# Performance work log

Measured on AMD Instinct MI355X. Metric: run time of the kernel, lower is better.

Reference implementation:

```python
import jax, jax.numpy as jnp
import numpy as np

TAU = 2.0
BN_EPS = 1e-5
HEADS = 8

# spikingjelly-style Heaviside spike with sigmoid surrogate gradient (alpha=4)
@jax.custom_vjp
def spike(x):
    return (x >= 0.0).astype(x.dtype)

def _spike_fwd(x):
    return (x >= 0.0).astype(x.dtype), x

def _spike_bwd(x, g):
    s = jax.nn.sigmoid(4.0 * x)
    return (g * 4.0 * s * (1.0 - s),)

spike.defvjp(_spike_fwd, _spike_bwd)

def lif(x, thresh):
    """Multi-step LIF (tau=2, decay_input=True, hard reset to 0, detach_reset).
    x: (T, ...) input current; returns spikes of the same shape."""
    def step(v, xt):
        v = v + (xt - v) / TAU          # charge
        s = spike(v - thresh)           # fire
        v = v * (1.0 - jax.lax.stop_gradient(s))  # hard reset, detached
        return v, s
    _, s = jax.lax.scan(step, jnp.zeros_like(x[0]), x)
    return s

def bn(x, gamma, beta, mean, var):
    # inference-mode BatchNorm2d over channel axis 2 of (T,B,C,H,W)
    sh = (1, 1, -1, 1, 1)
    scale = gamma / jnp.sqrt(var + BN_EPS)
    return (x - mean.reshape(sh)) * scale.reshape(sh) + beta.reshape(sh)

def setup_inputs() -> dict:
    key = jax.random.key(0)
    T, B, C, H, W = 4, 16, 512, 16, 16
    ks = jax.random.split(key, 24)
    def wmat(k):
        return jax.random.normal(k, (C, C), jnp.float32) * (1.0 / np.sqrt(C))
    def bnp(k):
        k1, k2, k3, k4 = jax.random.split(k, 4)
        return (jax.random.normal(k1, (C,), jnp.float32) * 0.1 + 1.0,
                jax.random.normal(k2, (C,), jnp.float32) * 0.1,
                jax.random.normal(k3, (C,), jnp.float32) * 0.1,
                jax.random.uniform(k4, (C,), jnp.float32) + 0.5)
    qg, qb, qm, qvar = bnp(ks[1]); kg, kb, km, kvar = bnp(ks[3])
    vg, vb, vm, vvar = bnp(ks[5]); pg, pb, pm, pvar = bnp(ks[8])
    return {
        'x': jax.random.normal(ks[0], (T, B, C, H, W), jnp.float32),
        'wq': wmat(ks[10]), 'qg': qg, 'qb': qb, 'qm': qm, 'qvar': qvar,
        'wk': wmat(ks[11]), 'kg': kg, 'kb': kb, 'km': km, 'kvar': kvar,
        'wv': wmat(ks[12]), 'vg': vg, 'vb': vb, 'vm': vm, 'vvar': vvar,
        'wp': wmat(ks[13]), 'bp': jax.random.normal(ks[14], (C,), jnp.float32) * 0.02,
        'pg': pg, 'pb': pb, 'pm': pm, 'pvar': pvar,
    }

def reference(x, wq, qg, qb, qm, qvar, wk, kg, kb, km, kvar,
              wv, vg, vb, vm, vvar, wp, bp, pg, pb, pm, pvar):
    T, B, C, H, W = x.shape
    dh = C // HEADS
    N = H * W
    identity = x
    xs = lif(x, 1.0)  # shortcut_lif

    def branch(w, g, b, m, v):
        y = jnp.einsum('tbchw,oc->tbohw', xs, w)  # 1x1 conv, no bias
        return lif(bn(y, g, b, m, v), 1.0)

    # (T,B,C,H,W) spikes -> (T,B,heads,N,dh)
    def to_heads(s):
        return s.reshape(T, B, HEADS, dh, N).transpose(0, 1, 2, 4, 3)

    q = to_heads(branch(wq, qg, qb, qm, qvar))
    k = to_heads(branch(wk, kg, kb, km, kvar))
    v = to_heads(branch(wv, vg, vb, vm, vvar))

    kv = (k * v).sum(axis=3, keepdims=True)   # sum over tokens N -> (T,B,h,1,dh)
    kv = lif(kv, 0.5)                          # talking_heads_lif (v_threshold=0.5)

    out = q * kv                               # (T,B,h,N,dh)
    out = out.transpose(0, 1, 2, 4, 3).reshape(T, B, C, H, W)
    out = jnp.einsum('tbchw,oc->tbohw', out, wp) + bp.reshape(1, 1, -1, 1, 1)
    out = bn(out, pg, pb, pm, pvar) + identity
    return out, v
```

## Files before the change

### kernel.cpp

```cpp
#include <hip/hip_runtime.h>
#include <hip/hip_bf16.h>

typedef unsigned short u16;
typedef unsigned int u32;
typedef __attribute__((ext_vector_type(8))) short bh8;
typedef __attribute__((ext_vector_type(4))) short sh4;
typedef __attribute__((ext_vector_type(4))) float f4;

#define T_   4
#define B_   16
#define C_   512
#define N_   256
#define M2_  4096

__device__ __forceinline__ u16 f2bf(float f) {
  u32 u = __float_as_uint(f);
  u32 r = (u + 0x7FFFu + ((u >> 16) & 1u)) >> 16;
  return (u16)r;
}
__device__ __forceinline__ void gl_lds16(const void* g, void* l) {
  __builtin_amdgcn_global_load_lds(
      (const __attribute__((address_space(1))) unsigned int*)g,
      (__attribute__((address_space(3))) unsigned int*)l, 16, 0, 0);
}

__global__ void k_prep_lif(const float* __restrict__ x, u16* __restrict__ xs,
                           const float* __restrict__ wq, const float* __restrict__ wk,
                           const float* __restrict__ wv, const float* __restrict__ wp,
                           const float* qg, const float* qb, const float* qm, const float* qv,
                           const float* kg, const float* kb, const float* km, const float* kv2,
                           const float* vg, const float* vb, const float* vm, const float* vv,
                           const float* pg, const float* pb, const float* pm, const float* pv,
                           const float* bp,
                           u16* __restrict__ wcat, u16* __restrict__ wpcat,
                           float* bns, float* pss) {
  __shared__ u16 sp[4][64][68];
  int bid = blockIdx.x;
  int tid = threadIdx.x;
  if (bid < 512) {
    int b = bid >> 5, c0 = ((bid >> 2) & 7) * 64, n0 = (bid & 3) * 64;
    int rq = tid >> 4;
    int n4 = (tid & 15) * 4;
    float v[16];
#pragma unroll
    for (int i = 0; i < 16; i++) v[i] = 0.f;
    for (int t = 0; t < 4; t++) {
      const float* xb = x + (((size_t)t * 16 + b) * 512 + c0) * 256 + n0;
#pragma unroll
      for (int i = 0; i < 4; i++) {
        int row = rq + i * 16;
        f4 xv = *(const f4*)(xb + (size_t)row * 256 + n4);
        sh4 sv;
#pragma unroll
        for (int j = 0; j < 4; j++) {
          float vv2 = v[i * 4 + j];
          vv2 = vv2 + (xv[j] - vv2) * 0.5f;
          u16 s = 0;
          if (vv2 >= 1.0f) { s = 0x3F80; vv2 = 0.f; }
          v[i * 4 + j] = vv2;
          sv[j] = (short)s;
        }
        *(sh4*)&sp[t][row][n4] = sv;
      }
    }
    __syncthreads();
    int cp = (tid & 31) * 2;
    int nq = tid >> 5;
    for (int t = 0; t < 4; t++) {
      u16* ob = xs + (((size_t)t * 16 + b) * 256 + n0) * 512 + c0;
#pragma unroll
      for (int i = 0; i < 8; i++) {
        int n = nq + i * 8;
        u32 w = (u32)sp[t][cp][n] | ((u32)sp[t][cp + 1][n] << 16);
        *(u32*)(ob + (size_t)n * 512 + cp) = w;
      }
    }
  } else {
    int id = (bid - 512) * 256 + tid;
    if (id < 1048576) {
      int mat = id >> 18;
      int rc  = id & 262143;
      int o = rc >> 9, c = rc & 511;
      const float* src = (mat == 0) ? wq : (mat == 1) ? wk : (mat == 2) ? wv : wp;
      float w = src[rc];
      u16 hu = f2bf(w);
      float hf = __uint_as_float(((u32)hu) << 16);
      u16 lu = f2bf(w - hf);
      if (mat < 3) {
        size_t base = ((size_t)(mat * 512 + o)) * 1024 + c;
        wcat[base] = hu; wcat[base + 512] = lu;
      } else {
        size_t base = (size_t)o * 1024 + c;
        wpcat[base] = hu; wpcat[base + 512] = lu;
      }
    } else {
      int j = id - 1048576;
      if (j < 1536) {
        int br = j >> 9, c = j & 511;
        const float *g, *b, *m, *va;
        if (br == 0)      { g = qg; b = qb; m = qm; va = qv; }
        else if (br == 1) { g = kg; b = kb; m = km; va = kv2; }
        else              { g = vg; b = vb; m = vm; va = vv; }
        float s = g[c] / sqrtf(va[c] + 1e-5f);
        bns[j * 4 + 0] = s; bns[j * 4 + 1] = m[c]; bns[j * 4 + 2] = b[c];
        bns[j * 4 + 3] = 0.f;
      } else if (j < 2048) {
        int c = j - 1536;
        float s = pg[c] / sqrtf(pv[c] + 1e-5f);
        pss[c * 4 + 0] = bp[c]; pss[c * 4 + 1] = pm[c];
        pss[c * 4 + 2] = s;     pss[c * 4 + 3] = pb[c];
      }
    }
  }
}

__launch_bounds__(256, 2)
__global__ void k_qkv_gemm(const u16* __restrict__ xs, const u16* __restrict__ wcat,
                           const float* __restrict__ bns,
                           u16* __restrict__ qs, u16* __restrict__ kvsp) {
  __shared__ char lds[81920];
  int tid = threadIdx.x, lane = tid & 63, wid = tid >> 6;
  int wr = wid >> 1, wc = wid & 1, lr = lane & 15, lq = lane >> 4;
  int m0 = blockIdx.x * 128, o0 = blockIdx.y * 96;

  float scl[3], mn[3], bt[3];
#pragma unroll
  for (int ni = 0; ni < 3; ni++) {
    int ch = o0 + wc * 48 + ni * 16 + lr;
    scl[ni] = bns[ch * 4]; mn[ni] = bns[ch * 4 + 1]; bt[ni] = bns[ch * 4 + 2];
  }

  int srow = tid >> 3;
  u32 sgoff = (u32)(((tid & 7) ^ (srow & 7)) << 4);
  u32 ldst = (u32)tid * 16;

  u32 aoff[4], boff[3];
#pragma unroll
  for (int mi = 0; mi < 4; mi++) {
    int r = wr * 64 + mi * 16 + lr;
    aoff[mi] = r * 128 + ((lq ^ (r & 7)) << 4);
  }
#pragma unroll
  for (int ni = 0; ni < 3; ni++) {
    int r = wc * 48 + ni * 16 + lr;
    boff[ni] = r * 128 + ((lq ^ (r & 7)) << 4);
  }

  const char* Bb = (const char*)wcat + (size_t)o0 * 2048;

  auto STAGE = [&](int buf, int step) {
    int t = step >> 3;
    u32 kb = (u32)(step & 7) * 128;
    const char* Ab = (const char*)xs + ((size_t)t * M2_ + m0) * 1024;
    char* L = lds + buf * 40960;
#pragma unroll
    for (int r2 = 0; r2 < 4; r2++)
      gl_lds16(Ab + (size_t)(r2 * 32 + srow) * 1024 + kb + sgoff, L + r2 * 4096 + ldst);
#pragma unroll
    for (int r2 = 0; r2 < 3; r2++) {
      gl_lds16(Bb + (size_t)(r2 * 32 + srow) * 2048 + kb + sgoff, L + 16384 + r2 * 4096 + ldst);
      gl_lds16(Bb + (size_t)(r2 * 32 + srow) * 2048 + 1024 + kb + sgoff, L + 28672 + r2 * 4096 + ldst);
    }
  };

  float vst[4][3][4];
#pragma unroll
  for (int a = 0; a < 4; a++)
#pragma unroll
    for (int b = 0; b < 3; b++)
#pragma unroll
      for (int c = 0; c < 4; c++) vst[a][b][c] = 0.f;

  f4 acc[4][3];
  STAGE(0, 0);
  __syncthreads();
  int cur = 0;
  for (int step = 0; step < 32; ++step) {
    int ks = step & 7;
    if (ks == 0) {
#pragma unroll
      for (int a = 0; a < 4; a++)
#pragma unroll
        for (int b = 0; b < 3; b++) { acc[a][b][0] = 0.f; acc[a][b][1] = 0.f; acc[a][b][2] = 0.f; acc[a][b][3] = 0.f; }
    }
    if (step < 31) STAGE(cur ^ 1, step + 1);
    const char* L = lds + cur * 40960;
#pragma unroll
    for (int h = 0; h < 2; h++) {
      u32 hx = (u32)h << 6;
      bh8 af[4], bf[3], lf[3];
#pragma unroll
      for (int mi = 0; mi < 4; mi++)
        af[mi] = *(const bh8*)(L + (aoff[mi] ^ hx));
#pragma unroll
      for (int ni = 0; ni < 3; ni++) {
        bf[ni] = *(const bh8*)(L + 16384 + (boff[ni] ^ hx));
        lf[ni] = *(const bh8*)(L + 28672 + (boff[ni] ^ hx));
      }
#pragma unroll
      for (int mi = 0; mi < 4; mi++)
#pragma unroll
        for (int ni = 0; ni < 3; ni++)
          acc[mi][ni] = __builtin_amdgcn_mfma_f32_16x16x32_bf16(af[mi], bf[ni], acc[mi][ni], 0, 0, 0);
#pragma unroll
      for (int mi = 0; mi < 4; mi++)
#pragma unroll
        for (int ni = 0; ni < 3; ni++)
          acc[mi][ni] = __builtin_amdgcn_mfma_f32_16x16x32_bf16(af[mi], lf[ni], acc[mi][ni], 0, 0, 0);
    }
    asm volatile("s_waitcnt vmcnt(0)" ::: "memory");
    __builtin_amdgcn_s_barrier();
    cur ^= 1;
    if (ks == 7) {
      int t = step >> 3;
#pragma unroll
      for (int mi = 0; mi < 4; mi++)
#pragma unroll
        for (int ni = 0; ni < 3; ni++)
#pragma unroll
          for (int j = 0; j < 4; j++) {
            float y = acc[mi][ni][j];
            y = (y - mn[ni]) * scl[ni] + bt[ni];
            float vv = vst[mi][ni][j];
            vv = vv + (y - vv) * 0.5f;
            u16 s = 0;
            if (vv >= 1.0f) { s = 0x3F80; vv = 0.f; }
            vst[mi][ni][j] = vv;
            int rg = m0 + wr * 64 + mi * 16 + lq * 4 + j;
            int o = o0 + wc * 48 + ni * 16 + lr;
            size_t rowg = (size_t)t * M2_ + rg;
            if (o < 512) qs[rowg * 512 + o] = s;
            else         kvsp[rowg * 1024 + (o - 512)] = s;
          }
    }
  }
}

__global__ void k_kvv(const u16* __restrict__ kvsp, float* __restrict__ vout,
                      int* __restrict__ kvp) {
  int tb = blockIdx.x >> 3, nc = blockIdx.x & 7;
  int tid = threadIdx.x;
  const char* base = (const char*)kvsp + ((size_t)tb * 256 + nc * 32) * 2048;
  int c = tid * 2, h = c >> 6, d = c & 63;
  float* vo = vout + (((size_t)tb * 8 + h) * 256 + nc * 32) * 64 + d;
  int cnt0 = 0, cnt1 = 0;
  for (int n = 0; n < 32; n++) {
    u32 kk = *(const u32*)(base + (size_t)n * 2048 + c * 2);
    u32 vv = *(const u32*)(base + (size_t)n * 2048 + 1024 + c * 2);
    u32 a = kk & vv;
    cnt0 += (a & 0xFFFFu) ? 1 : 0;
    cnt1 += (a >> 16) ? 1 : 0;
    float2 w;
    w.x = (vv & 0xFFFFu) ? 1.f : 0.f;
    w.y = (vv >> 16) ? 1.f : 0.f;
    *(float2*)(vo + (size_t)n * 64) = w;
  }
  kvp[((tb * 8 + nc) << 9) + c]     = cnt0;
  kvp[((tb * 8 + nc) << 9) + c + 1] = cnt1;
}

__global__ void k_tlif(const int* __restrict__ kvp, unsigned char* __restrict__ mask) {
  int id = blockIdx.x * 256 + threadIdx.x;
  int b = id >> 9, c = id & 511;
  float v = 0.f;
  for (int t = 0; t < 4; t++) {
    int tb = t * 16 + b;
    int s = 0;
#pragma unroll
    for (int nc = 0; nc < 8; nc++) s += kvp[((tb * 8 + nc) << 9) + c];
    float xx = (float)s;
    v = v + (xx - v) * 0.5f;
    unsigned char sp = 0;
    if (v >= 0.5f) { sp = 1; v = 0.f; }
    mask[tb * 512 + c] = sp;
  }
}

__launch_bounds__(256, 2)
__global__ void k_proj_gemm(const u16* __restrict__ qs, const unsigned char* __restrict__ mask,
                            const u16* __restrict__ wpc, const float* __restrict__ pss,
                            const float* __restrict__ x, float* __restrict__ out) {
  __shared__ char lds[66560];
  u16* lm = (u16*)(lds + 65536);
  int tid = threadIdx.x, lane = tid & 63, wid = tid >> 6;
  int wr = wid >> 1, wc = wid & 1, lr = lane & 15, lq = lane >> 4;
  int m0 = blockIdx.x * 128, o0 = blockIdx.y * 64;
  int tb = m0 >> 8;

  lm[tid]       = mask[tb * 512 + tid]       ? (u16)0xFFFF : (u16)0;
  lm[tid + 256] = mask[tb * 512 + tid + 256] ? (u16)0xFFFF : (u16)0;

  int srow = tid >> 3;
  u32 sgoff = (u32)(((tid & 7) ^ (srow & 7)) << 4);
  u32 ldst = (u32)tid * 16;

  u32 aoff[4], boff[2];
#pragma unroll
  for (int mi = 0; mi < 4; mi++) {
    int r = wr * 64 + mi * 16 + lr;
    aoff[mi] = r * 128 + ((lq ^ (r & 7)) << 4);
  }
#pragma unroll
  for (int ni = 0; ni < 2; ni++) {
    int r = wc * 32 + ni * 16 + lr;
    boff[ni] = r * 128 + ((lq ^ (r & 7)) << 4);
  }

  const char* Ab = (const char*)qs + (size_t)m0 * 1024;
  const char* Bb = (const char*)wpc + (size_t)o0 * 2048;

  auto STAGE = [&](int buf, int step) {
    u32 kb = (u32)step * 128;
    char* L = lds + buf * 32768;
#pragma unroll
    for (int r2 = 0; r2 < 4; r2++)
      gl_lds16(Ab + (size_t)(r2 * 32 + srow) * 1024 + kb + sgoff, L + r2 * 4096 + ldst);
#pragma unroll
    for (int r2 = 0; r2 < 2; r2++) {
      gl_lds16(Bb + (size_t)(r2 * 32 + srow) * 2048 + kb + sgoff, L + 16384 + r2 * 4096 + ldst);
      gl_lds16(Bb + (size_t)(r2 * 32 + srow) * 2048 + 1024 + kb + sgoff, L + 24576 + r2 * 4096 + ldst);
    }
  };

  f4 acc[4][2];
#pragma unroll
  for (int a = 0; a < 4; a++)
#pragma unroll
    for (int b = 0; b < 2; b++) { acc[a][b][0] = 0.f; acc[a][b][1] = 0.f; acc[a][b][2] = 0.f; acc[a][b][3] = 0.f; }

  STAGE(0, 0);
  __syncthreads();
  int cur = 0;
  for (int step = 0; step < 8; ++step) {
    u32 kb = (u32)step * 128;
    if (step < 7) STAGE(cur ^ 1, step + 1);
    const char* L = lds + cur * 32768;
#pragma unroll
    for (int h = 0; h < 2; h++) {
      u32 hx = (u32)h << 6;
      bh8 mq = *(const bh8*)((const char*)lm + kb + (h << 6) + lq * 16);
      bh8 af[4], bf[2], lf[2];
#pragma unroll
      for (int mi = 0; mi < 4; mi++) {
        af[mi] = *(const bh8*)(L + (aoff[mi] ^ hx));
        af[mi] = af[mi] & mq;
      }
#pragma unroll
      for (int ni = 0; ni < 2; ni++) {
        bf[ni] = *(const bh8*)(L + 16384 + (boff[ni] ^ hx));
        lf[ni] = *(const bh8*)(L + 24576 + (boff[ni] ^ hx));
      }
#pragma unroll
      for (int mi = 0; mi < 4; mi++)
#pragma unroll
        for (int ni = 0; ni < 2; ni++)
          acc[mi][ni] = __builtin_amdgcn_mfma_f32_16x16x32_bf16(af[mi], bf[ni], acc[mi][ni], 0, 0, 0);
#pragma unroll
      for (int mi = 0; mi < 4; mi++)
#pragma unroll
        for (int ni = 0; ni < 2; ni++)
          acc[mi][ni] = __builtin_amdgcn_mfma_f32_16x16x32_bf16(af[mi], lf[ni], acc[mi][ni], 0, 0, 0);
    }
    asm volatile("s_waitcnt vmcnt(0)" ::: "memory");
    __builtin_amdgcn_s_barrier();
    cur ^= 1;
  }
#pragma unroll
  for (int mi = 0; mi < 4; mi++)
#pragma unroll
    for (int ni = 0; ni < 2; ni++) {
      int o = o0 + wc * 32 + ni * 16 + lr;
      f4 ps = *(const f4*)&pss[o * 4];
      int n = (m0 & 255) + wr * 64 + mi * 16 + lq * 4;
      size_t idx = (size_t)tb * 131072 + (size_t)o * 256 + n;
      f4 xv = *(const f4*)&x[idx];
      f4 res;
#pragma unroll
      for (int j = 0; j < 4; j++) {
        float u = acc[mi][ni][j] + ps[0];
        u = (u - ps[1]) * ps[2] + ps[3];
        res[j] = u + xv[j];
      }
      *(f4*)&out[idx] = res;
    }
}

extern "C" void kernel_launch(void* const* d_in, const int* in_sizes, int n_in,
                              void* d_out, int out_size, void* d_ws, size_t ws_size,
                              hipStream_t stream) {
  const float* x  = (const float*)d_in[0];
  const float* wq = (const float*)d_in[1];
  const float* qg = (const float*)d_in[2];
  const float* qb = (const float*)d_in[3];
  const float* qm = (const float*)d_in[4];
  const float* qv = (const float*)d_in[5];
  const float* wk = (const float*)d_in[6];
  const float* kg = (const float*)d_in[7];
  const float* kb = (const float*)d_in[8];
  const float* km = (const float*)d_in[9];
  const float* kv = (const float*)d_in[10];
  const float* wv = (const float*)d_in[11];
  const float* vg = (const float*)d_in[12];
  const float* vb = (const float*)d_in[13];
  const float* vm = (const float*)d_in[14];
  const float* vv = (const float*)d_in[15];
  const float* wp = (const float*)d_in[16];
  const float* bp = (const float*)d_in[17];
  const float* pg = (const float*)d_in[18];
  const float* pb = (const float*)d_in[19];
  const float* pm = (const float*)d_in[20];
  const float* pv = (const float*)d_in[21];

  char* w = (char*)d_ws;
  u16*  XS    = (u16*)(w + 0);
  u16*  QS    = (u16*)(w + 16777216);
  u16*  KVSP  = (u16*)(w + 33554432);
  u16*  WCAT  = (u16*)(w + 67108864);
  u16*  WPCAT = (u16*)(w + 70254592);
  float* BNS  = (float*)(w + 71303168);
  float* PSS  = (float*)(w + 71327744);
  int*   KVP  = (int*)(w + 71335936);
  unsigned char* MASK = (unsigned char*)(w + 72384512);

  float* out  = (float*)d_out;
  float* vout = out + 8388608;

  k_prep_lif<<<4616, 256, 0, stream>>>(x, XS, wq, wk, wv, wp,
                                       qg, qb, qm, qv, kg, kb, km, kv,
                                       vg, vb, vm, vv, pg, pb, pm, pv, bp,
                                       WCAT, WPCAT, BNS, PSS);
  k_qkv_gemm<<<dim3(32, 16), 256, 0, stream>>>(XS, WCAT, BNS, QS, KVSP);
  k_kvv<<<512, 256, 0, stream>>>(KVSP, vout, KVP);
  k_tlif<<<32, 256, 0, stream>>>(KVP, MASK);
  k_proj_gemm<<<dim3(128, 8), 256, 0, stream>>>(QS, MASK, WPCAT, PSS, x, out);
}
```

Before: 213.7 us.

## Fuse k*v token reduction and v output into QKV GEMM epilogue

Result: faster. 203.2 us (-4.9%).

```diff
diff --git a/kernel.cpp b/kernel.cpp
--- a/kernel.cpp
+++ b/kernel.cpp
@@ -41,20 +41,27 @@
     int b = bid >> 5, c0 = ((bid >> 2) & 7) * 64, n0 = (bid & 3) * 64;
     int rq = tid >> 4;
     int n4 = (tid & 15) * 4;
-    float v[16];
-#pragma unroll
-    for (int i = 0; i < 16; i++) v[i] = 0.f;
+    f4 xr[4][4];
+#pragma unroll
     for (int t = 0; t < 4; t++) {
       const float* xb = x + (((size_t)t * 16 + b) * 512 + c0) * 256 + n0;
 #pragma unroll
+      for (int i = 0; i < 4; i++)
+        xr[t][i] = *(const f4*)(xb + (size_t)(rq + i * 16) * 256 + n4);
+    }
+    float v[16];
+#pragma unroll
+    for (int i = 0; i < 16; i++) v[i] = 0.f;
+#pragma unroll
+    for (int t = 0; t < 4; t++) {
+#pragma unroll
       for (int i = 0; i < 4; i++) {
         int row = rq + i * 16;
-        f4 xv = *(const f4*)(xb + (size_t)row * 256 + n4);
         sh4 sv;
 #pragma unroll
         for (int j = 0; j < 4; j++) {
           float vv2 = v[i * 4 + j];
-          vv2 = vv2 + (xv[j] - vv2) * 0.5f;
+          vv2 = vv2 + (xr[t][i][j] - vv2) * 0.5f;
           u16 s = 0;
           if (vv2 >= 1.0f) { s = 0x3F80; vv2 = 0.f; }
           v[i * 4 + j] = vv2;
@@ -87,7 +94,8 @@
       float hf = __uint_as_float(((u32)hu) << 16);
       u16 lu = f2bf(w - hf);
       if (mat < 3) {
-        size_t base = ((size_t)(mat * 512 + o)) * 1024 + c;
+        int rI = (o >> 5) * 96 + mat * 32 + (o & 31);
+        size_t base = (size_t)rI * 1024 + c;
         wcat[base] = hu; wcat[base + 512] = lu;
       } else {
         size_t base = (size_t)o * 1024 + c;
@@ -96,14 +104,15 @@
     } else {
       int j = id - 1048576;
       if (j < 1536) {
-        int br = j >> 9, c = j & 511;
+        int br = j >> 9, o = j & 511;
         const float *g, *b, *m, *va;
         if (br == 0)      { g = qg; b = qb; m = qm; va = qv; }
         else if (br == 1) { g = kg; b = kb; m = km; va = kv2; }
         else              { g = vg; b = vb; m = vm; va = vv; }
-        float s = g[c] / sqrtf(va[c] + 1e-5f);
-        bns[j * 4 + 0] = s; bns[j * 4 + 1] = m[c]; bns[j * 4 + 2] = b[c];
-        bns[j * 4 + 3] = 0.f;
+        float s = g[o] / sqrtf(va[o] + 1e-5f);
+        int rI = (o >> 5) * 96 + br * 32 + (o & 31);
+        bns[rI * 4 + 0] = s; bns[rI * 4 + 1] = m[o]; bns[rI * 4 + 2] = b[o];
+        bns[rI * 4 + 3] = 0.f;
       } else if (j < 2048) {
         int c = j - 1536;
         float s = pg[c] / sqrtf(pv[c] + 1e-5f);
@@ -117,32 +126,37 @@
 __launch_bounds__(256, 2)
 __global__ void k_qkv_gemm(const u16* __restrict__ xs, const u16* __restrict__ wcat,
                            const float* __restrict__ bns,
-                           u16* __restrict__ qs, u16* __restrict__ kvsp) {
+                           u16* __restrict__ qs, float* __restrict__ vout,
+                           int* __restrict__ kvp) {
   __shared__ char lds[81920];
-  int tid = threadIdx.x, lane = tid & 63, wid = tid >> 6;
-  int wr = wid >> 1, wc = wid & 1, lr = lane & 15, lq = lane >> 4;
-  int m0 = blockIdx.x * 128, o0 = blockIdx.y * 96;
-
-  float scl[3], mn[3], bt[3];
-#pragma unroll
-  for (int ni = 0; ni < 3; ni++) {
-    int ch = o0 + wc * 48 + ni * 16 + lr;
-    scl[ni] = bns[ch * 4]; mn[ni] = bns[ch * 4 + 1]; bt[ni] = bns[ch * 4 + 2];
+  int tid = threadIdx.x, lane = tid & 63;
+  int wr = tid >> 6;
+  int lr = lane & 15, lq = lane >> 4;
+  int m0 = blockIdx.x * 128;
+  int cb = blockIdx.y;
+  int o0 = cb * 96;
+  int b = m0 >> 8, n0 = m0 & 255, half = (m0 >> 7) & 1;
+
+  float scl[6], mn[6], bt[6];
+#pragma unroll
+  for (int ni = 0; ni < 6; ni++) {
+    int rI = o0 + ni * 16 + lr;
+    scl[ni] = bns[rI * 4]; mn[ni] = bns[rI * 4 + 1]; bt[ni] = bns[rI * 4 + 2];
   }
 
   int srow = tid >> 3;
   u32 sgoff = (u32)(((tid & 7) ^ (srow & 7)) << 4);
   u32 ldst = (u32)tid * 16;
 
-  u32 aoff[4], boff[3];
-#pragma unroll
-  for (int mi = 0; mi < 4; mi++) {
-    int r = wr * 64 + mi * 16 + lr;
+  u32 aoff[2], boff[6];
+#pragma unroll
+  for (int mi = 0; mi < 2; mi++) {
+    int r = wr * 32 + mi * 16 + lr;
     aoff[mi] = r * 128 + ((lq ^ (r & 7)) << 4);
   }
 #pragma unroll
-  for (int ni = 0; ni < 3; ni++) {
-    int r = wc * 48 + ni * 16 + lr;
+  for (int ni = 0; ni < 6; ni++) {
+    int r = ni * 16 + lr;
     boff[ni] = r * 128 + ((lq ^ (r & 7)) << 4);
   }
 
@@ -163,15 +177,15 @@
     }
   };
 
-  float vst[4][3][4];
-#pragma unroll
-  for (int a = 0; a < 4; a++)
-#pragma unroll
-    for (int b = 0; b < 3; b++)
-#pragma unroll
-      for (int c = 0; c < 4; c++) vst[a][b][c] = 0.f;
-
-  f4 acc[4][3];
+  float vst[2][6][4];
+#pragma unroll
+  for (int a = 0; a < 2; a++)
+#pragma unroll
+    for (int bq = 0; bq < 6; bq++)
+#pragma unroll
+      for (int c = 0; c < 4; c++) vst[a][bq][c] = 0.f;
+
+  f4 acc[2][6];
   STAGE(0, 0);
   __syncthreads();
   int cur = 0;
@@ -179,33 +193,33 @@
     int ks = step & 7;
     if (ks == 0) {
 #pragma unroll
-      for (int a = 0; a < 4; a++)
-#pragma unroll
-        for (int b = 0; b < 3; b++) { acc[a][b][0] = 0.f; acc[a][b][1] = 0.f; acc[a][b][2] = 0.f; acc[a][b][3] = 0.f; }
+      for (int a = 0; a < 2; a++)
+#pragma unroll
+        for (int bq = 0; bq < 6; bq++) { acc[a][bq][0] = 0.f; acc[a][bq][1] = 0.f; acc[a][bq][2] = 0.f; acc[a][bq][3] = 0.f; }
     }
     if (step < 31) STAGE(cur ^ 1, step + 1);
     const char* L = lds + cur * 40960;
 #pragma unroll
     for (int h = 0; h < 2; h++) {
       u32 hx = (u32)h << 6;
-      bh8 af[4], bf[3], lf[3];
-#pragma unroll
-      for (int mi = 0; mi < 4; mi++)
+      bh8 af[2], bf[6], lf[6];
+#pragma unroll
+      for (int mi = 0; mi < 2; mi++)
         af[mi] = *(const bh8*)(L + (aoff[mi] ^ hx));
 #pragma unroll
-      for (int ni = 0; ni < 3; ni++) {
+      for (int ni = 0; ni < 6; ni++) {
         bf[ni] = *(const bh8*)(L + 16384 + (boff[ni] ^ hx));
         lf[ni] = *(const bh8*)(L + 28672 + (boff[ni] ^ hx));
       }
 #pragma unroll
-      for (int mi = 0; mi < 4; mi++)
-#pragma unroll
-        for (int ni = 0; ni < 3; ni++)
+      for (int mi = 0; mi < 2; mi++)
+#pragma unroll
+        for (int ni = 0; ni < 6; ni++)
           acc[mi][ni] = __builtin_amdgcn_mfma_f32_16x16x32_bf16(af[mi], bf[ni], acc[mi][ni], 0, 0, 0);
 #pragma unroll
-      for (int mi = 0; mi < 4; mi++)
-#pragma unroll
-        for (int ni = 0; ni < 3; ni++)
+      for (int mi = 0; mi < 2; mi++)
+#pragma unroll
+        for (int ni = 0; ni < 6; ni++)
           acc[mi][ni] = __builtin_amdgcn_mfma_f32_16x16x32_bf16(af[mi], lf[ni], acc[mi][ni], 0, 0, 0);
     }
     asm volatile("s_waitcnt vmcnt(0)" ::: "memory");
@@ -213,50 +227,69 @@
     cur ^= 1;
     if (ks == 7) {
       int t = step >> 3;
-#pragma unroll
-      for (int mi = 0; mi < 4; mi++)
-#pragma unroll
-        for (int ni = 0; ni < 3; ni++)
+      unsigned char* vbuf = (unsigned char*)(lds + (cur ^ 1) * 40960);
+      short* cbuf = (short*)(lds + (cur ^ 1) * 40960 + 4096);
+      int cnt0 = 0, cnt1 = 0;
+      u16 kbits[2]; kbits[0] = 0; kbits[1] = 0;
+#pragma unroll
+      for (int ni = 0; ni < 6; ni++) {
+#pragma unroll
+        for (int mi = 0; mi < 2; mi++) {
 #pragma unroll
           for (int j = 0; j < 4; j++) {
-            float y = acc[mi][ni][j];
-            y = (y - mn[ni]) * scl[ni] + bt[ni];
+            float y = (acc[mi][ni][j] - mn[ni]) * scl[ni] + bt[ni];
             float vv = vst[mi][ni][j];
             vv = vv + (y - vv) * 0.5f;
-            u16 s = 0;
-            if (vv >= 1.0f) { s = 0x3F80; vv = 0.f; }
+            int s = (vv >= 1.0f) ? 1 : 0;
+            if (s) vv = 0.f;
             vst[mi][ni][j] = vv;
-            int rg = m0 + wr * 64 + mi * 16 + lq * 4 + j;
-            int o = o0 + wc * 48 + ni * 16 + lr;
-            size_t rowg = (size_t)t * M2_ + rg;
-            if (o < 512) qs[rowg * 512 + o] = s;
-            else         kvsp[rowg * 1024 + (o - 512)] = s;
+            int jj = ni & 1;
+            if (ni < 2) {
+              int rg = m0 + wr * 32 + mi * 16 + lq * 4 + j;
+              int cc = cb * 32 + jj * 16 + lr;
+              qs[((size_t)t * M2_ + rg) * 512 + cc] = s ? (u16)0x3F80 : (u16)0;
+            } else if (ni < 4) {
+              kbits[mi] |= (u16)(s << (jj * 4 + j));
+            } else {
+              int row = wr * 32 + mi * 16 + lq * 4 + j;
+              vbuf[row * 32 + jj * 16 + lr] = (unsigned char)s;
+              int kbit = (kbits[mi] >> (jj * 4 + j)) & 1;
+              if (jj == 0) cnt0 += (s & kbit); else cnt1 += (s & kbit);
+            }
           }
-    }
-  }
-}
-
-__global__ void k_kvv(const u16* __restrict__ kvsp, float* __restrict__ vout,
-                      int* __restrict__ kvp) {
-  int tb = blockIdx.x >> 3, nc = blockIdx.x & 7;
-  int tid = threadIdx.x;
-  const char* base = (const char*)kvsp + ((size_t)tb * 256 + nc * 32) * 2048;
-  int c = tid * 2, h = c >> 6, d = c & 63;
-  float* vo = vout + (((size_t)tb * 8 + h) * 256 + nc * 32) * 64 + d;
-  int cnt0 = 0, cnt1 = 0;
-  for (int n = 0; n < 32; n++) {
-    u32 kk = *(const u32*)(base + (size_t)n * 2048 + c * 2);
-    u32 vv = *(const u32*)(base + (size_t)n * 2048 + 1024 + c * 2);
-    u32 a = kk & vv;
-    cnt0 += (a & 0xFFFFu) ? 1 : 0;
-    cnt1 += (a >> 16) ? 1 : 0;
-    float2 w;
-    w.x = (vv & 0xFFFFu) ? 1.f : 0.f;
-    w.y = (vv >> 16) ? 1.f : 0.f;
-    *(float2*)(vo + (size_t)n * 64) = w;
-  }
-  kvp[((tb * 8 + nc) << 9) + c]     = cnt0;
-  kvp[((tb * 8 + nc) << 9) + c + 1] = cnt1;
+        }
+      }
+      cbuf[tid * 2] = (short)cnt0; cbuf[tid * 2 + 1] = (short)cnt1;
+      asm volatile("s_waitcnt lgkmcnt(0)" ::: "memory");
+      __builtin_amdgcn_s_barrier();
+      __builtin_amdgcn_sched_barrier(0);
+      {
+        int d0 = (cb & 1) * 32;
+        int hh = cb >> 1;
+        float* vo = vout + (((size_t)(t * 16 + b) * 8 + hh) * 256 + n0) * 64 + d0;
+#pragma unroll
+        for (int p = 0; p < 4; p++) {
+          int row = (tid >> 3) + p * 32;
+          const unsigned char* src = vbuf + row * 32 + (tid & 7) * 4;
+          f4 w2; w2[0] = src[0]; w2[1] = src[1]; w2[2] = src[2]; w2[3] = src[3];
+          *(f4*)(vo + (size_t)row * 64 + (tid & 7) * 4) = w2;
+        }
+        if (tid < 32) {
+          int lr2 = tid & 15, jj = tid >> 4;
+          int ssum = 0;
+#pragma unroll
+          for (int w3 = 0; w3 < 4; w3++)
+#pragma unroll
+            for (int q3 = 0; q3 < 4; q3++)
+              ssum += cbuf[(w3 * 64 + q3 * 16 + lr2) * 2 + jj];
+          kvp[(((t * 16 + b) * 2 + half) << 9) + cb * 32 + jj * 16 + lr2] = ssum;
+        }
+      }
+      asm volatile("s_waitcnt lgkmcnt(0)" ::: "memory");
+      __builtin_amdgcn_s_barrier();
+      __builtin_amdgcn_sched_barrier(0);
+    }
+  }
 }
 
 __global__ void k_tlif(const int* __restrict__ kvp, unsigned char* __restrict__ mask) {
@@ -265,9 +298,7 @@
   float v = 0.f;
   for (int t = 0; t < 4; t++) {
     int tb = t * 16 + b;
-    int s = 0;
-#pragma unroll
-    for (int nc = 0; nc < 8; nc++) s += kvp[((tb * 8 + nc) << 9) + c];
+    int s = kvp[((tb * 2) << 9) + c] + kvp[((tb * 2 + 1) << 9) + c];
     float xx = (float)s;
     v = v + (xx - v) * 0.5f;
     unsigned char sp = 0;
@@ -326,7 +357,7 @@
 #pragma unroll
   for (int a = 0; a < 4; a++)
 #pragma unroll
-    for (int b = 0; b < 2; b++) { acc[a][b][0] = 0.f; acc[a][b][1] = 0.f; acc[a][b][2] = 0.f; acc[a][b][3] = 0.f; }
+    for (int b2 = 0; b2 < 2; b2++) { acc[a][b2][0] = 0.f; acc[a][b2][1] = 0.f; acc[a][b2][2] = 0.f; acc[a][b2][3] = 0.f; }
 
   STAGE(0, 0);
   __syncthreads();
@@ -414,13 +445,12 @@
   char* w = (char*)d_ws;
   u16*  XS    = (u16*)(w + 0);
   u16*  QS    = (u16*)(w + 16777216);
-  u16*  KVSP  = (u16*)(w + 33554432);
-  u16*  WCAT  = (u16*)(w + 67108864);
-  u16*  WPCAT = (u16*)(w + 70254592);
-  float* BNS  = (float*)(w + 71303168);
-  float* PSS  = (float*)(w + 71327744);
-  int*   KVP  = (int*)(w + 71335936);
-  unsigned char* MASK = (unsigned char*)(w + 72384512);
+  u16*  WCAT  = (u16*)(w + 33554432);
+  u16*  WPCAT = (u16*)(w + 36700160);
+  float* BNS  = (float*)(w + 37748736);
+  float* PSS  = (float*)(w + 37773312);
+  int*   KVP  = (int*)(w + 37781504);
+  unsigned char* MASK = (unsigned char*)(w + 38043648);
 
   float* out  = (float*)d_out;
   float* vout = out + 8388608;
@@ -429,8 +459,7 @@
                                        qg, qb, qm, qv, kg, kb, km, kv,
                                        vg, vb, vm, vv, pg, pb, pm, pv, bp,
                                        WCAT, WPCAT, BNS, PSS);
-  k_qkv_gemm<<<dim3(32, 16), 256, 0, stream>>>(XS, WCAT, BNS, QS, KVSP);
-  k_kvv<<<512, 256, 0, stream>>>(KVSP, vout, KVP);
+  k_qkv_gemm<<<dim3(32, 16), 256, 0, stream>>>(XS, WCAT, BNS, QS, vout, KVP);
   k_tlif<<<32, 256, 0, stream>>>(KVP, MASK);
   k_proj_gemm<<<dim3(128, 8), 256, 0, stream>>>(QS, MASK, WPCAT, PSS, x, out);
 }
```
